# Kernel optimization log

Hardware: AMD Instinct MI355X
Metric: run time of the kernel (lower is better)

## Reference

```python
import jax, jax.numpy as jnp
import numpy as np

PADDING_INDEX = 999
RESOLUTION = 0.25
SUBSAMPLING = 2
RES_LOW = RESOLUTION * SUBSAMPLING          # 0.5 A / voxel (low-res grid)
GRID_DIM_LOW = 64 // SUBSAMPLING            # 32 voxel crop
ATOMIC_RADIUS = 0.5
RADIUS_SCALE = float(np.sqrt(SUBSAMPLING))
N_CHANNELS = 5
CUBES_AROUND = 5
LATO = 2 * CUBES_AROUND + 1                 # 11


def setup_inputs() -> dict:
    key = jax.random.key(0)
    k1, k2 = jax.random.split(key)
    B, L = 32, 512
    coords = jax.random.uniform(k1, (B, L, 3), jnp.float32, -10.0, 10.0)
    atoms_channel = jax.random.randint(k2, (B, L), 0, N_CHANNELS).astype(jnp.int32)
    radius = jnp.full((B, L), ATOMIC_RADIUS, jnp.float32)
    return {"coords": coords, "atoms_channel": atoms_channel, "radius": radius}


def _standard_cube():
    # [lato, lato, lato, 3] integer offsets -d..d (as float for arithmetic)
    g = jnp.arange(-CUBES_AROUND, CUBES_AROUND + 1, dtype=jnp.float32)
    gx, gy, gz = jnp.meshgrid(g, g, g, indexing="ij")
    return jnp.stack([gx, gy, gz], axis=-1)


def reference(coords, atoms_channel, radius):
    B, L, _ = coords.shape
    res = RES_LOW
    # ---- FieldMaker._add_dumb_coords: append +/- sentinel atoms to center molecule ----
    dumb = jnp.abs(coords).max() + 10.0
    dumb_rep = jnp.broadcast_to(dumb, (B, 1, 3))
    coords = jnp.concatenate([coords, -dumb_rep, dumb_rep], axis=1)          # [B, L+2, 3]
    atoms_channel = jnp.concatenate(
        [atoms_channel, jnp.zeros((B, 2), atoms_channel.dtype)], axis=1)
    radius = jnp.concatenate(
        [radius, jnp.full((B, 2), ATOMIC_RADIUS, radius.dtype)], axis=1) * RADIUS_SCALE
    L2 = L + 2

    # ---- Voxels.forward ----
    mincoords = jnp.trunc(coords.min(axis=1) / res)                          # [B, 3]
    # data-dependent box size (concrete Python ints, as in the torch module)
    maxc = np.asarray(coords.reshape(-1, 3).max(axis=0))
    minm = np.asarray(mincoords.min(axis=0))
    box = [int(np.ceil(maxc[i] / res) - minm[i] + LATO) for i in range(3)]

    translation = (mincoords - CUBES_AROUND)[:, None, :]                     # [B,1,3]
    coords_t = coords / res - translation                                    # [B,L2,3], >= 0
    radius_t = radius / res                                                  # [B,L2]
    disc = jnp.trunc(coords_t)                                               # voxel base index

    cube = _standard_cube()                                                  # [l,l,l,3]
    # voxel-center positions probed by each atom: [B,L2,l,l,l,3]
    centers = disc[:, :, None, None, None, :] + cube + 1.0 + 0.5 * res
    dist = jnp.linalg.norm(coords_t[:, :, None, None, None, :] - centers, axis=-1)
    exponent = dist ** 2 / (0.93 ** 2 * radius_t[:, :, None, None, None] ** 2)
    exp_mask = exponent >= 10.0
    vol_cubes = jnp.exp(-jnp.where(exp_mask, 10.0, exponent))
    # torch drops masked entries from the scatter -> contribute exactly 0 in log space
    vals = jnp.where(exp_mask, 0.0, jnp.log1p(-vol_cubes))                   # [B,L2,l,l,l]

    idx = (disc[:, :, None, None, None, :] + cube + 1.0).astype(jnp.int32)   # [B,L2,l,l,l,3]
    b_idx = jnp.broadcast_to(jnp.arange(B, dtype=jnp.int32)[:, None, None, None, None],
                             (B, L2, LATO, LATO, LATO))
    c_idx = jnp.broadcast_to(atoms_channel.astype(jnp.int32)[:, :, None, None, None],
                             (B, L2, LATO, LATO, LATO))

    volume = jnp.zeros((B, box[0] + 1, box[1] + 1, box[2] + 1, N_CHANNELS), coords.dtype)
    volume = volume.at[b_idx.reshape(-1),
                       idx[..., 0].reshape(-1),
                       idx[..., 1].reshape(-1),
                       idx[..., 2].reshape(-1),
                       c_idx.reshape(-1)].add(vals.reshape(-1))
    volume = 1.0 - jnp.exp(volume)
    volume = jnp.transpose(volume, (0, 4, 1, 2, 3))                          # [B,C,X,Y,Z]

    # ---- FieldMaker crop to central low-res grid ----
    c = volume.shape[-1] // 2
    lo, hi = c - GRID_DIM_LOW // 2, c + GRID_DIM_LOW // 2
    return volume[:, :, lo:hi, lo:hi, lo:hi]
```

## Files before the change

### kernel.cpp

```cpp
#include <hip/hip_runtime.h>
#include <math.h>

#define BATCH 32
#define LSEQ  512
#define NCH   5
#define GRID  32
#define CA    5
#define LATO  11
#define NPAIR 121
#define XS    2
#define SLABS (GRID / XS)
#define TPB   512
#define VOXB  (XS * NCH * GRID * GRID)

__global__ void __launch_bounds__(TPB) fused_fieldmaker(
        const float* __restrict__ coords,
        const int*   __restrict__ chan,
        const float* __restrict__ radius,
        float*       __restrict__ out) {
    __shared__ float  vol[VOXB];
    __shared__ float4 alist[LSEQ];
    __shared__ int    ameta[LSEQ];
    __shared__ int    s_cnt;
    __shared__ float  s_T, s_lo;

    const int tid = threadIdx.x;
    const int b   = blockIdx.x / SLABS;
    const int xs  = blockIdx.x - b * SLABS;
    const int x0  = xs * XS;

    float m = 0.0f;
    const float4* c4 = (const float4*)coords;
    for (int i = tid; i < BATCH * LSEQ * 3 / 4; i += TPB) {
        float4 v = c4[i];
        m = fmaxf(m, fmaxf(fmaxf(fabsf(v.x), fabsf(v.y)),
                           fmaxf(fabsf(v.z), fabsf(v.w))));
    }
    vol[tid] = m;
    __syncthreads();
    for (int w = TPB / 2; w >= 64; w >>= 1) {
        if (tid < w) vol[tid] = fmaxf(vol[tid], vol[tid + w]);
        __syncthreads();
    }
    if (tid < 64) {
        float mm = vol[tid];
        #pragma unroll
        for (int off = 32; off > 0; off >>= 1)
            mm = fmaxf(mm, __shfl_down(mm, off));
        if (tid == 0) {
            float D  = mm + 10.0f;
            float mf = truncf(-D * 2.0f);
            int box  = (int)ceilf(D * 2.0f) - (int)mf + LATO;
            int lo   = (box + 1) / 2 - GRID / 2;
            s_T  = mf - (float)CA;
            s_lo = (float)lo;
            s_cnt = 0;
        }
    }
    __syncthreads();
    const float T   = s_T;
    const float flo = s_lo;

    for (int i = tid; i < VOXB; i += TPB) vol[i] = 0.0f;
    __syncthreads();

    for (int l = tid; l < LSEQ; l += TPB) {
        int base = (b * LSEQ + l) * 3;
        float tx = coords[base + 0] * 2.0f - T;
        float ty = coords[base + 1] * 2.0f - T;
        float tz = coords[base + 2] * 2.0f - T;
        float ux = tx - flo, uy = ty - flo, uz = tz - flo;
        int fxi = (int)floorf(ux);
        int fyi = (int)floorf(uy);
        int fzi = (int)floorf(uz);
        bool ok = (fxi >= x0 - 6) && (fxi <= x0 + XS + 4)
               && (fyi >= -6) && (fyi <= 35)
               && (fzi >= -6) && (fzi <= 35);
        if (ok) {
            float r  = radius[b * LSEQ + l] * 1.41421356f;
            float rt = r * 2.0f;
            float denom = 0.8649f * (rt * rt);
            int slot = atomicAdd(&s_cnt, 1);
            alist[slot] = make_float4(ux, uy, uz, denom);
            ameta[slot] = (chan[b * LSEQ + l] << 8) | (fxi + 64);
        }
    }
    __syncthreads();

    const int cnt   = s_cnt;
    const int ntask = cnt * NPAIR;
    for (int t = tid; t < ntask; t += TPB) {
        int a = t / NPAIR;
        int p = t - a * NPAIR;
        int oy = p / LATO;
        int oz = p - oy * LATO;

        float4 A  = alist[a];
        int meta  = ameta[a];
        int fxi   = (meta & 255) - 64;
        int ch    = meta >> 8;
        float den = A.w;

        int fyi = (int)floorf(A.y);
        int fzi = (int)floorf(A.z);
        int gy  = fyi + oy - 4;
        int gz  = fzi + oz - 4;
        if ((unsigned)gy >= GRID || (unsigned)gz >= GRID) continue;

        float dy  = (A.y - 0.25f) - (float)gy;
        float dz  = (A.z - 0.25f) - (float)gz;
        float dyz = dy * dy + dz * dz;
        if (dyz >= 10.0f * den) continue;

        float rx    = A.x - 0.25f;
        int   lbase = (gy << 5) + gz;
        #pragma unroll
        for (int s = 0; s < XS; ++s) {
            int gx = x0 + s;
            int od = gx - fxi;
            if (od < -4 || od > 6) continue;
            float dx = rx - (float)gx;
            float e  = (dx * dx + dyz) / den;
            if (e < 10.0f) {
                float val = __logf(1.0f - __expf(-e));
                atomicAdd(&vol[(s * NCH + ch) * 1024 + lbase], val);
            }
        }
    }
    __syncthreads();

    for (int i = tid; i < VOXB; i += TPB) {
        int s   = i / (NCH * 1024);
        int rem = i - s * (NCH * 1024);
        int c   = rem >> 10;
        int yz  = rem & 1023;
        out[(((size_t)b * NCH + c) * GRID + (x0 + s)) * 1024 + yz] =
            1.0f - __expf(vol[i]);
    }
}

extern "C" void kernel_launch(void* const* d_in, const int* in_sizes, int n_in,
                              void* d_out, int out_size, void* d_ws, size_t ws_size,
                              hipStream_t stream) {
    const float* coords = (const float*)d_in[0];
    const int*   chan   = (const int*)d_in[1];
    const float* radius = (const float*)d_in[2];
    float* out = (float*)d_out;

    fused_fieldmaker<<<BATCH * SLABS, TPB, 0, stream>>>(coords, chan, radius, out);
}
```

Measured before the change: 98.01 us.

## Split global max into a separate kernel and give each block one x-slice

Each block previously recomputed the global abs-max over all coordinates. That reduction now runs once in a small pre-kernel using atomicMax into workspace, after a memset. Blocks now own a single x-plane instead of two. Each atom's x-distance term is precomputed and atoms whose x contribution already exceeds the cutoff are culled up front. The y/z stencil shrinks to 9x9, shared memory rows are padded to 33, and output is written as float4. The cost is two extra launches and twice as many blocks, each of which reloads the atom list.

```diff
diff --git a/kernel.cpp b/kernel.cpp
--- a/kernel.cpp
+++ b/kernel.cpp
@@ -5,137 +5,109 @@
 #define LSEQ  512
 #define NCH   5
 #define GRID  32
-#define CA    5
-#define LATO  11
-#define NPAIR 121
-#define XS    2
-#define SLABS (GRID / XS)
 #define TPB   512
-#define VOXB  (XS * NCH * GRID * GRID)
+#define NPAIR 81
+#define ROWS  33
+#define CHSZ  (ROWS * 32)
+#define VOXB  (NCH * CHSZ)
+
+__global__ void __launch_bounds__(256) max_kernel(const float4* __restrict__ c4,
+                                                  unsigned* __restrict__ slot) {
+    int i = blockIdx.x * 256 + threadIdx.x;
+    float4 v = c4[i];
+    float m = fmaxf(fmaxf(fabsf(v.x), fabsf(v.y)), fmaxf(fabsf(v.z), fabsf(v.w)));
+    #pragma unroll
+    for (int off = 32; off > 0; off >>= 1)
+        m = fmaxf(m, __shfl_down(m, off));
+    if ((threadIdx.x & 63) == 0)
+        atomicMax(slot, __float_as_uint(m));
+}
 
 __global__ void __launch_bounds__(TPB) fused_fieldmaker(
         const float* __restrict__ coords,
         const int*   __restrict__ chan,
         const float* __restrict__ radius,
+        const unsigned* __restrict__ slot,
         float*       __restrict__ out) {
     __shared__ float  vol[VOXB];
     __shared__ float4 alist[LSEQ];
     __shared__ int    ameta[LSEQ];
     __shared__ int    s_cnt;
-    __shared__ float  s_T, s_lo;
 
     const int tid = threadIdx.x;
-    const int b   = blockIdx.x / SLABS;
-    const int xs  = blockIdx.x - b * SLABS;
-    const int x0  = xs * XS;
+    const int b   = blockIdx.x >> 5;
+    const int gx  = blockIdx.x & 31;
 
-    float m = 0.0f;
-    const float4* c4 = (const float4*)coords;
-    for (int i = tid; i < BATCH * LSEQ * 3 / 4; i += TPB) {
-        float4 v = c4[i];
-        m = fmaxf(m, fmaxf(fmaxf(fabsf(v.x), fabsf(v.y)),
-                           fmaxf(fabsf(v.z), fabsf(v.w))));
-    }
-    vol[tid] = m;
-    __syncthreads();
-    for (int w = TPB / 2; w >= 64; w >>= 1) {
-        if (tid < w) vol[tid] = fmaxf(vol[tid], vol[tid + w]);
-        __syncthreads();
-    }
-    if (tid < 64) {
-        float mm = vol[tid];
-        #pragma unroll
-        for (int off = 32; off > 0; off >>= 1)
-            mm = fmaxf(mm, __shfl_down(mm, off));
-        if (tid == 0) {
-            float D  = mm + 10.0f;
-            float mf = truncf(-D * 2.0f);
-            int box  = (int)ceilf(D * 2.0f) - (int)mf + LATO;
-            int lo   = (box + 1) / 2 - GRID / 2;
-            s_T  = mf - (float)CA;
-            s_lo = (float)lo;
-            s_cnt = 0;
-        }
-    }
-    __syncthreads();
-    const float T   = s_T;
-    const float flo = s_lo;
+    float amax = __uint_as_float(*slot);
+    float D  = amax + 10.0f;
+    float mf = truncf(-D * 2.0f);
+    int box  = (int)ceilf(D * 2.0f) - (int)mf + 11;
+    int lo   = (box + 1) / 2 - GRID / 2;
+    float Tl = (mf - 5.0f) + (float)lo;
 
-    for (int i = tid; i < VOXB; i += TPB) vol[i] = 0.0f;
+    float4* vol4 = (float4*)vol;
+    for (int i = tid; i < VOXB / 4; i += TPB)
+        vol4[i] = make_float4(0.f, 0.f, 0.f, 0.f);
+    if (tid == 0) s_cnt = 0;
     __syncthreads();
 
-    for (int l = tid; l < LSEQ; l += TPB) {
-        int base = (b * LSEQ + l) * 3;
-        float tx = coords[base + 0] * 2.0f - T;
-        float ty = coords[base + 1] * 2.0f - T;
-        float tz = coords[base + 2] * 2.0f - T;
-        float ux = tx - flo, uy = ty - flo, uz = tz - flo;
-        int fxi = (int)floorf(ux);
+    {
+        int base = (b * LSEQ + tid) * 3;
+        float ux = coords[base + 0] * 2.0f - Tl;
+        float uy = coords[base + 1] * 2.0f - Tl;
+        float uz = coords[base + 2] * 2.0f - Tl;
         int fyi = (int)floorf(uy);
         int fzi = (int)floorf(uz);
-        bool ok = (fxi >= x0 - 6) && (fxi <= x0 + XS + 4)
-               && (fyi >= -6) && (fyi <= 35)
-               && (fzi >= -6) && (fzi <= 35);
-        if (ok) {
-            float r  = radius[b * LSEQ + l] * 1.41421356f;
-            float rt = r * 2.0f;
-            float denom = 0.8649f * (rt * rt);
-            int slot = atomicAdd(&s_cnt, 1);
-            alist[slot] = make_float4(ux, uy, uz, denom);
-            ameta[slot] = (chan[b * LSEQ + l] << 8) | (fxi + 64);
+
+        float r   = radius[b * LSEQ + tid] * 1.41421356f;
+        float rt  = r * 2.0f;
+        float den = 0.8649f * (rt * rt);
+        float inv = 1.0f / den;
+
+        float dx = ux - 0.25f - (float)gx;
+        float ex = dx * dx * inv;
+
+        if (ex < 10.0f && fyi >= -5 && fyi <= 36 && fzi >= -5 && fzi <= 36) {
+            int slotl = atomicAdd(&s_cnt, 1);
+            alist[slotl] = make_float4(ex, uy - 0.25f, uz - 0.25f, inv);
+            ameta[slotl] = (fyi + 12) | ((fzi + 12) << 8)
+                         | (chan[b * LSEQ + tid] << 16);
         }
     }
     __syncthreads();
 
-    const int cnt   = s_cnt;
-    const int ntask = cnt * NPAIR;
+    const int ntask = s_cnt * NPAIR;
     for (int t = tid; t < ntask; t += TPB) {
-        int a = t / NPAIR;
-        int p = t - a * NPAIR;
-        int oy = p / LATO;
-        int oz = p - oy * LATO;
+        unsigned a = (unsigned)t / NPAIR;
+        unsigned p = (unsigned)t - a * NPAIR;
+        unsigned oy = p / 9u;
+        unsigned oz = p - oy * 9u;
 
-        float4 A  = alist[a];
-        int meta  = ameta[a];
-        int fxi   = (meta & 255) - 64;
-        int ch    = meta >> 8;
-        float den = A.w;
+        float4 A = alist[a];
+        int meta = ameta[a];
+        int gy = (meta & 255) - 16 + (int)oy;
+        int gz = ((meta >> 8) & 255) - 16 + (int)oz;
+        if ((unsigned)gy >= 32u || (unsigned)gz >= 32u) continue;
 
-        int fyi = (int)floorf(A.y);
-        int fzi = (int)floorf(A.z);
-        int gy  = fyi + oy - 4;
-        int gz  = fzi + oz - 4;
-        if ((unsigned)gy >= GRID || (unsigned)gz >= GRID) continue;
-
-        float dy  = (A.y - 0.25f) - (float)gy;
-        float dz  = (A.z - 0.25f) - (float)gz;
-        float dyz = dy * dy + dz * dz;
-        if (dyz >= 10.0f * den) continue;
-
-        float rx    = A.x - 0.25f;
-        int   lbase = (gy << 5) + gz;
-        #pragma unroll
-        for (int s = 0; s < XS; ++s) {
-            int gx = x0 + s;
-            int od = gx - fxi;
-            if (od < -4 || od > 6) continue;
-            float dx = rx - (float)gx;
-            float e  = (dx * dx + dyz) / den;
-            if (e < 10.0f) {
-                float val = __logf(1.0f - __expf(-e));
-                atomicAdd(&vol[(s * NCH + ch) * 1024 + lbase], val);
-            }
+        float dy  = A.y - (float)gy;
+        float dz  = A.z - (float)gz;
+        float e   = A.x + (dy * dy + dz * dz) * A.w;
+        if (e < 10.0f) {
+            float val = __logf(1.0f - __expf(-e));
+            atomicAdd(&vol[(meta >> 16) * CHSZ + gy * ROWS + gz], val);
         }
     }
     __syncthreads();
 
-    for (int i = tid; i < VOXB; i += TPB) {
-        int s   = i / (NCH * 1024);
-        int rem = i - s * (NCH * 1024);
-        int c   = rem >> 10;
-        int yz  = rem & 1023;
-        out[(((size_t)b * NCH + c) * GRID + (x0 + s)) * 1024 + yz] =
-            1.0f - __expf(vol[i]);
+    for (int i = tid; i < NCH * 256; i += TPB) {
+        int c   = i >> 8;
+        int r4  = i & 255;
+        int gy  = r4 >> 3;
+        int gz0 = (r4 & 7) << 2;
+        const float* v = &vol[c * CHSZ + gy * ROWS + gz0];
+        float4 o = make_float4(1.0f - __expf(v[0]), 1.0f - __expf(v[1]),
+                               1.0f - __expf(v[2]), 1.0f - __expf(v[3]));
+        ((float4*)out)[(((size_t)b * NCH + c) * GRID + gx) * 256 + r4] = o;
     }
 }
 
@@ -146,6 +118,9 @@
     const int*   chan   = (const int*)d_in[1];
     const float* radius = (const float*)d_in[2];
     float* out = (float*)d_out;
+    unsigned* slot = (unsigned*)d_ws;
 
-    fused_fieldmaker<<<BATCH * SLABS, TPB, 0, stream>>>(coords, chan, radius, out);
+    hipMemsetAsync(slot, 0, 4, stream);
+    max_kernel<<<48, 256, 0, stream>>>((const float4*)coords, slot);
+    fused_fieldmaker<<<BATCH * GRID, TPB, 0, stream>>>(coords, chan, radius, slot, out);
 }
```

After: 86.80 us. -11.4%, faster.
